# Performance work log

Measured on AMD Instinct MI355X. Metric: run time of the kernel, lower is better.

The kernel has to match this reference:

```python
import jax, jax.numpy as jnp
import numpy as np

USER_SIZE = 1_000_000
ITEM_SIZE = 1_000_000
EMBED = 64
BATCH = 4096
NUM_TOTAL = 100
STD = 0.01


def setup_inputs() -> dict:
    key = jax.random.key(0)
    ks = jax.random.split(key, 16)
    d = {}
    d["user"] = jax.random.randint(ks[0], (BATCH, 1), 0, USER_SIZE, dtype=jnp.int64 if jax.config.jax_enable_x64 else jnp.int32)
    d["item"] = jax.random.randint(ks[1], (BATCH, NUM_TOTAL), 0, ITEM_SIZE, dtype=jnp.int64 if jax.config.jax_enable_x64 else jnp.int32)
    d["num_total"] = NUM_TOTAL
    # Embedding tables stored as [vocab, embed] (transpose of nn.Linear weight [embed, vocab])
    d["Wu_gmf"] = jax.random.normal(ks[2], (USER_SIZE, EMBED), jnp.float32) * STD
    d["bu_gmf"] = jnp.zeros((EMBED,), jnp.float32)
    d["Wu_mlp"] = jax.random.normal(ks[3], (USER_SIZE, EMBED), jnp.float32) * STD
    d["bu_mlp"] = jnp.zeros((EMBED,), jnp.float32)
    d["Wi_gmf"] = jax.random.normal(ks[4], (ITEM_SIZE, EMBED), jnp.float32) * STD
    d["bi_gmf"] = jnp.zeros((EMBED,), jnp.float32)
    d["Wi_mlp"] = jax.random.normal(ks[5], (ITEM_SIZE, EMBED), jnp.float32) * STD
    d["bi_mlp"] = jnp.zeros((EMBED,), jnp.float32)
    # MLP tower, stored as [in, out]
    d["W1"] = jax.random.normal(ks[6], (2 * EMBED, 2 * EMBED), jnp.float32) * STD
    d["b1"] = jnp.zeros((2 * EMBED,), jnp.float32)
    d["W2"] = jax.random.normal(ks[7], (2 * EMBED, EMBED), jnp.float32) * STD
    d["b2"] = jnp.zeros((EMBED,), jnp.float32)
    d["W3"] = jax.random.normal(ks[8], (EMBED, EMBED // 2), jnp.float32) * STD
    d["b3"] = jnp.zeros((EMBED // 2,), jnp.float32)
    d["Wp"] = jax.random.normal(ks[9], (3 * EMBED // 2, 1), jnp.float32) * STD
    d["bp"] = jnp.zeros((1,), jnp.float32)
    return d


def reference(user, item, num_total, Wu_gmf, bu_gmf, Wu_mlp, bu_mlp, Wi_gmf, bi_gmf, Wi_mlp, bi_mlp, W1, b1, W2, b2, W3, b3, Wp, bp):
    # one-hot @ Linear == embedding gather (column select of weight) + bias
    eu_g = Wu_gmf[user[:, 0]] + bu_gmf              # [B, E]
    eu_m = Wu_mlp[user[:, 0]] + bu_mlp              # [B, E]
    ei_g = Wi_gmf[item] + bi_gmf                    # [B, N, E]
    ei_m = Wi_mlp[item] + bi_mlp                    # [B, N, E]

    gmf = eu_g[:, None, :] * ei_g                   # [B, N, E]

    eu_m_b = jnp.broadcast_to(eu_m[:, None, :], ei_m.shape)
    inter = jnp.concatenate([eu_m_b, ei_m], axis=2)  # [B, N, 2E]
    h1 = jax.nn.relu(inter @ W1 + b1)
    h2 = jax.nn.relu(h1 @ W2 + b2)
    h3 = jax.nn.relu(h2 @ W3 + b3)                  # [B, N, E/2]

    concat = jnp.concatenate([gmf, h3], axis=2)     # [B, N, 3E/2]
    pred = jax.nn.sigmoid(concat @ Wp + bp)         # [B, N, 1]
    return pred[..., 0]                             # [B, N]
```

## Files before the change

kernel.cpp:

```cpp
#include <hip/hip_runtime.h>


typedef __attribute__((ext_vector_type(8))) short bf16x8;
typedef __attribute__((ext_vector_type(4))) float f32x4;

__device__ __forceinline__ short f2bf(float x){
  unsigned u = __float_as_uint(x);
  u += 0x7fffu + ((u >> 16) & 1u);
  return (short)(u >> 16);
}
__device__ __forceinline__ float bf2f(short s){
  return __uint_as_float(((unsigned)(unsigned short)s) << 16);
}

__global__ __launch_bounds__(256) void ncf_prep_w(
    const float* __restrict__ W1, const float* __restrict__ W2,
    const float* __restrict__ W3, short* __restrict__ ws)
{
  int i = blockIdx.x * 256 + threadIdx.x;
  if (i < 8192){
    int col = i >> 6, k = i & 63;
    ws[i] = f2bf(W1[(64 + k)*128 + col]);
  } else if (i < 16384){
    int t = i - 8192; int col = t >> 7, k = t & 127;
    ws[i] = f2bf(W2[k*64 + col]);
  } else if (i < 18432){
    int t = i - 16384; int col = t >> 6, k = t & 63;
    ws[i] = f2bf(W3[k*32 + col]);
  }
}

__global__ __launch_bounds__(128) void ncf_prep_u(
    const int* __restrict__ user,
    const float* __restrict__ Wu_gmf, const float* __restrict__ bu_gmf,
    const float* __restrict__ Wu_mlp, const float* __restrict__ bu_mlp,
    const float* __restrict__ bi_gmf, const float* __restrict__ bi_mlp,
    const float* __restrict__ W1, const float* __restrict__ b1,
    const float* __restrict__ Wp,
    float* __restrict__ Xu, float* __restrict__ wup, float* __restrict__ cu,
    int B)
{
  int b = blockIdx.x; if (b >= B) return;
  int j = threadIdx.x;
  long u = (long)user[b];
  float acc = b1[j];
  #pragma unroll 4
  for (int k = 0; k < 64; k++){
    float eu = Wu_mlp[u*64 + k] + bu_mlp[k];
    acc += eu * W1[k*128 + j] + bi_mlp[k] * W1[(64 + k)*128 + j];
  }
  Xu[b*128 + j] = acc;
  if (j < 64){
    float wg = (Wu_gmf[u*64 + j] + bu_gmf[j]) * Wp[j];
    wup[b*64 + j] = wg;
    float c = wg * bi_gmf[j];
    c += __shfl_xor(c, 1);  c += __shfl_xor(c, 2);
    c += __shfl_xor(c, 4);  c += __shfl_xor(c, 8);
    c += __shfl_xor(c, 16); c += __shfl_xor(c, 32);
    if (j == 0) cu[b] = c;
  }
}

__global__ __launch_bounds__(256) void ncf_main(
    const int* __restrict__ item,
    const float* __restrict__ Wi_mlp, const float* __restrict__ Wi_gmf,
    const short* __restrict__ W1iT, const short* __restrict__ W2T,
    const short* __restrict__ W3T,
    const float* __restrict__ b2, const float* __restrict__ b3,
    const float* __restrict__ Wp, const float* __restrict__ bp,
    const float* __restrict__ Xu, const float* __restrict__ wup,
    const float* __restrict__ cu,
    float* __restrict__ out, int N, int total)
{
  __shared__ __align__(16) short s_item[64][72];
  __shared__ __align__(16) short s_h1[64][136];
  __shared__ __align__(16) short s_h3[64][36];
  __shared__ int   s_bidx[64];
  __shared__ float s_pg[64];

  const int tid = threadIdx.x;
  const int p0  = blockIdx.x * 64;

  {
    int r = tid >> 2, q = tid & 3;
    int p = p0 + r; if (p >= total) p = total - 1;
    int b = p / N;
    long ib = (long)item[p] * 64;
    const float4* imp = (const float4*)(Wi_mlp + ib) + q*4;
    const float4* igp = (const float4*)(Wi_gmf + ib) + q*4;
    const float4* wq  = (const float4*)(wup + (long)b*64) + q*4;
    bf16x8 ia[2];
    float pg = 0.f;
    #pragma unroll
    for (int j = 0; j < 4; j++){
      float4 v = imp[j];
      float4 g = igp[j];
      float4 wv = wq[j];
      pg += g.x*wv.x + g.y*wv.y + g.z*wv.z + g.w*wv.w;
      int h = j >> 1, s = (j & 1) * 4;
      ia[h][s+0] = f2bf(v.x); ia[h][s+1] = f2bf(v.y);
      ia[h][s+2] = f2bf(v.z); ia[h][s+3] = f2bf(v.w);
    }
    *(bf16x8*)&s_item[r][q*16]     = ia[0];
    *(bf16x8*)&s_item[r][q*16 + 8] = ia[1];
    pg += __shfl_xor(pg, 1);
    pg += __shfl_xor(pg, 2);
    if (q == 0){ s_bidx[r] = b; s_pg[r] = pg + cu[b]; }
  }
  __syncthreads();

  const int w  = tid >> 6, l = tid & 63;
  const int lr = l & 15,  lg = l >> 4;

  {
    f32x4 acc[4][2];
    #pragma unroll
    for (int mt = 0; mt < 4; mt++)
      #pragma unroll
      for (int nt = 0; nt < 2; nt++)
        acc[mt][nt] = (f32x4){0.f, 0.f, 0.f, 0.f};
    #pragma unroll
    for (int ks = 0; ks < 2; ks++){
      bf16x8 af[4];
      #pragma unroll
      for (int mt = 0; mt < 4; mt++)
        af[mt] = *(const bf16x8*)&s_item[mt*16 + lr][ks*32 + lg*8];
      #pragma unroll
      for (int nt = 0; nt < 2; nt++){
        bf16x8 bfg = *(const bf16x8*)&W1iT[(w*32 + nt*16 + lr)*64 + ks*32 + lg*8];
        #pragma unroll
        for (int mt = 0; mt < 4; mt++)
          acc[mt][nt] = __builtin_amdgcn_mfma_f32_16x16x32_bf16(af[mt], bfg, acc[mt][nt], 0, 0, 0);
      }
    }
    #pragma unroll
    for (int nt = 0; nt < 2; nt++){
      int col = w*32 + nt*16 + lr;
      #pragma unroll
      for (int mt = 0; mt < 4; mt++)
        #pragma unroll
        for (int rr = 0; rr < 4; rr++){
          int row = mt*16 + lg*4 + rr;
          float v = acc[mt][nt][rr] + Xu[s_bidx[row]*128 + col];
          s_h1[row][col] = f2bf(v > 0.f ? v : 0.f);
        }
    }
  }
  __syncthreads();

  {
    f32x4 acc2[4];
    #pragma unroll
    for (int mt = 0; mt < 4; mt++) acc2[mt] = (f32x4){0.f, 0.f, 0.f, 0.f};
    #pragma unroll
    for (int ks = 0; ks < 4; ks++){
      bf16x8 bfg = *(const bf16x8*)&W2T[(w*16 + lr)*128 + ks*32 + lg*8];
      #pragma unroll
      for (int mt = 0; mt < 4; mt++){
        bf16x8 a = *(const bf16x8*)&s_h1[mt*16 + lr][ks*32 + lg*8];
        acc2[mt] = __builtin_amdgcn_mfma_f32_16x16x32_bf16(a, bfg, acc2[mt], 0, 0, 0);
      }
    }
    int col = w*16 + lr;
    float bb = b2[col];
    #pragma unroll
    for (int mt = 0; mt < 4; mt++)
      #pragma unroll
      for (int rr = 0; rr < 4; rr++){
        int row = mt*16 + lg*4 + rr;
        float v = acc2[mt][rr] + bb;
        s_item[row][col] = f2bf(v > 0.f ? v : 0.f);
      }
  }
  __syncthreads();

  if (w < 2){
    f32x4 acc3[4];
    #pragma unroll
    for (int mt = 0; mt < 4; mt++) acc3[mt] = (f32x4){0.f, 0.f, 0.f, 0.f};
    #pragma unroll
    for (int ks = 0; ks < 2; ks++){
      bf16x8 bfg = *(const bf16x8*)&W3T[(w*16 + lr)*64 + ks*32 + lg*8];
      #pragma unroll
      for (int mt = 0; mt < 4; mt++){
        bf16x8 a = *(const bf16x8*)&s_item[mt*16 + lr][ks*32 + lg*8];
        acc3[mt] = __builtin_amdgcn_mfma_f32_16x16x32_bf16(a, bfg, acc3[mt], 0, 0, 0);
      }
    }
    int col = w*16 + lr;
    float bb = b3[col];
    #pragma unroll
    for (int mt = 0; mt < 4; mt++)
      #pragma unroll
      for (int rr = 0; rr < 4; rr++){
        int row = mt*16 + lg*4 + rr;
        float v = acc3[mt][rr] + bb;
        s_h3[row][col] = f2bf(v > 0.f ? v : 0.f);
      }
  }
  __syncthreads();

  {
    int r = tid >> 2, q = tid & 3;
    float sum = 0.f;
    #pragma unroll
    for (int i = 0; i < 8; i++){
      int c = q*8 + i;
      sum += bf2f(s_h3[r][c]) * Wp[64 + c];
    }
    sum += __shfl_xor(sum, 1);
    sum += __shfl_xor(sum, 2);
    int p = p0 + r;
    if (q == 0 && p < total){
      float z = s_pg[r] + sum + bp[0];
      out[p] = 1.f / (1.f + __expf(-z));
    }
  }
}

extern "C" void kernel_launch(void* const* d_in, const int* in_sizes, int n_in,
                              void* d_out, int out_size, void* d_ws, size_t ws_size,
                              hipStream_t stream)
{
  const int*   user   = (const int*)  d_in[0];
  const int*   item   = (const int*)  d_in[1];
  const float* Wu_gmf = (const float*)d_in[3];
  const float* bu_gmf = (const float*)d_in[4];
  const float* Wu_mlp = (const float*)d_in[5];
  const float* bu_mlp = (const float*)d_in[6];
  const float* Wi_gmf = (const float*)d_in[7];
  const float* bi_gmf = (const float*)d_in[8];
  const float* Wi_mlp = (const float*)d_in[9];
  const float* bi_mlp = (const float*)d_in[10];
  const float* W1     = (const float*)d_in[11];
  const float* b1     = (const float*)d_in[12];
  const float* W2     = (const float*)d_in[13];
  const float* b2     = (const float*)d_in[14];
  const float* W3     = (const float*)d_in[15];
  const float* b3     = (const float*)d_in[16];
  const float* Wp     = (const float*)d_in[17];
  const float* bp     = (const float*)d_in[18];

  int B     = in_sizes[0];
  int total = in_sizes[1];
  int N     = total / B;

  short* W1iT = (short*)d_ws;
  short* W2T  = W1iT + 8192;
  short* W3T  = W2T  + 8192;
  float* Xu   = (float*)((char*)d_ws + 36864);
  float* wup  = Xu  + (size_t)B * 128;
  float* cuv  = wup + (size_t)B * 64;

  ncf_prep_w<<<72, 256, 0, stream>>>(W1, W2, W3, (short*)d_ws);
  ncf_prep_u<<<B, 128, 0, stream>>>(user, Wu_gmf, bu_gmf, Wu_mlp, bu_mlp,
                                    bi_gmf, bi_mlp, W1, b1, Wp,
                                    Xu, wup, cuv, B);

  int nblk = (total + 63) / 64;
  ncf_main<<<nblk, 256, 0, stream>>>(item, Wi_mlp, Wi_gmf,
      W1iT, W2T, W3T, b2, b3, Wp, bp, Xu, wup, cuv,
      (float*)d_out, N, total);
}
```

Measured before the change: 85.92 us.

## Use MFMA for user-side W1 projection, persistent main kernel with register-resident weights

The per-user W1 projection moves from a scalar loop (one block per user) to a 64-user-per-block MFMA tile. The constant bias term b1 + bi_mlp·W1 is folded into a single precomputed vector c1. The main kernel becomes persistent over 1024 blocks, loading the W1/W2/W3 fragments into registers once per block instead of once per tile. It also stages the (at most two) user Xu rows per tile into shared memory instead of reading Xu per element. This adds register pressure and a grid-stride loop with an extra barrier per tile. It also assumes B is a multiple of 64 and that a tile spans at most two users.

After: 85.60 us. Within noise of the previous version (-0.4%).

```diff
diff --git a/kernel.cpp b/kernel.cpp
--- a/kernel.cpp
+++ b/kernel.cpp
@@ -13,51 +13,116 @@
   return __uint_as_float(((unsigned)(unsigned short)s) << 16);
 }
 
+
 __global__ __launch_bounds__(256) void ncf_prep_w(
     const float* __restrict__ W1, const float* __restrict__ W2,
-    const float* __restrict__ W3, short* __restrict__ ws)
+    const float* __restrict__ W3, const float* __restrict__ b1,
+    const float* __restrict__ bi_mlp, short* __restrict__ ws,
+    float* __restrict__ c1)
 {
+  if (blockIdx.x == 104){
+    int j = threadIdx.x;
+    if (j < 128){
+      float acc = b1[j];
+      #pragma unroll 4
+      for (int k = 0; k < 64; k++)
+        acc += bi_mlp[k] * W1[(64 + k)*128 + j];
+      c1[j] = acc;
+    }
+    return;
+  }
   int i = blockIdx.x * 256 + threadIdx.x;
   if (i < 8192){
     int col = i >> 6, k = i & 63;
+    ws[i] = f2bf(W1[k*128 + col]);
+  } else if (i < 16384){
+    int t = i - 8192; int col = t >> 6, k = t & 63;
     ws[i] = f2bf(W1[(64 + k)*128 + col]);
-  } else if (i < 16384){
-    int t = i - 8192; int col = t >> 7, k = t & 127;
+  } else if (i < 24576){
+    int t = i - 16384; int col = t >> 7, k = t & 127;
     ws[i] = f2bf(W2[k*64 + col]);
-  } else if (i < 18432){
-    int t = i - 16384; int col = t >> 6, k = t & 63;
+  } else if (i < 26624){
+    int t = i - 24576; int col = t >> 6, k = t & 63;
     ws[i] = f2bf(W3[k*32 + col]);
   }
 }
 
-__global__ __launch_bounds__(128) void ncf_prep_u(
+__global__ __launch_bounds__(256) void ncf_prep_u(
     const int* __restrict__ user,
     const float* __restrict__ Wu_gmf, const float* __restrict__ bu_gmf,
     const float* __restrict__ Wu_mlp, const float* __restrict__ bu_mlp,
-    const float* __restrict__ bi_gmf, const float* __restrict__ bi_mlp,
-    const float* __restrict__ W1, const float* __restrict__ b1,
-    const float* __restrict__ Wp,
-    float* __restrict__ Xu, float* __restrict__ wup, float* __restrict__ cu,
-    int B)
+    const float* __restrict__ bi_gmf, const float* __restrict__ Wp,
+    const short* __restrict__ W1uT, const float* __restrict__ c1,
+    float* __restrict__ Xu, float* __restrict__ wup, float* __restrict__ cu)
 {
-  int b = blockIdx.x; if (b >= B) return;
-  int j = threadIdx.x;
+  __shared__ __align__(16) short s_eu[64][72];
+  const int tid = threadIdx.x;
+  const int r = tid >> 2, q = tid & 3;
+  const int b = blockIdx.x * 64 + r;
   long u = (long)user[b];
-  float acc = b1[j];
-  #pragma unroll 4
-  for (int k = 0; k < 64; k++){
-    float eu = Wu_mlp[u*64 + k] + bu_mlp[k];
-    acc += eu * W1[k*128 + j] + bi_mlp[k] * W1[(64 + k)*128 + j];
-  }
-  Xu[b*128 + j] = acc;
-  if (j < 64){
-    float wg = (Wu_gmf[u*64 + j] + bu_gmf[j]) * Wp[j];
-    wup[b*64 + j] = wg;
-    float c = wg * bi_gmf[j];
-    c += __shfl_xor(c, 1);  c += __shfl_xor(c, 2);
-    c += __shfl_xor(c, 4);  c += __shfl_xor(c, 8);
-    c += __shfl_xor(c, 16); c += __shfl_xor(c, 32);
-    if (j == 0) cu[b] = c;
+
+  {
+    const float4* ump = (const float4*)(Wu_mlp + u*64) + q*4;
+    const float4* bmp = (const float4*)(bu_mlp) + q*4;
+    const float4* ugp = (const float4*)(Wu_gmf + u*64) + q*4;
+    const float4* bgp = (const float4*)(bu_gmf) + q*4;
+    const float4* wpp = (const float4*)(Wp) + q*4;
+    const float4* bip = (const float4*)(bi_gmf) + q*4;
+    float4* wdst = (float4*)(wup + (long)b*64) + q*4;
+    bf16x8 ea[2];
+    float cacc = 0.f;
+    #pragma unroll
+    for (int j = 0; j < 4; j++){
+      float4 m = ump[j], mb = bmp[j];
+      int h = j >> 1, s = (j & 1) * 4;
+      ea[h][s+0] = f2bf(m.x + mb.x); ea[h][s+1] = f2bf(m.y + mb.y);
+      ea[h][s+2] = f2bf(m.z + mb.z); ea[h][s+3] = f2bf(m.w + mb.w);
+      float4 g = ugp[j], gb = bgp[j], wp = wpp[j], bi = bip[j];
+      float4 wg; wg.x = (g.x+gb.x)*wp.x; wg.y = (g.y+gb.y)*wp.y;
+                 wg.z = (g.z+gb.z)*wp.z; wg.w = (g.w+gb.w)*wp.w;
+      wdst[j] = wg;
+      cacc += wg.x*bi.x + wg.y*bi.y + wg.z*bi.z + wg.w*bi.w;
+    }
+    *(bf16x8*)&s_eu[r][q*16]     = ea[0];
+    *(bf16x8*)&s_eu[r][q*16 + 8] = ea[1];
+    cacc += __shfl_xor(cacc, 1);
+    cacc += __shfl_xor(cacc, 2);
+    if (q == 0) cu[b] = cacc;
+  }
+  __syncthreads();
+
+  const int w = tid >> 6, l = tid & 63, lr = l & 15, lg = l >> 4;
+  f32x4 acc[4][2];
+  #pragma unroll
+  for (int mt = 0; mt < 4; mt++)
+    #pragma unroll
+    for (int nt = 0; nt < 2; nt++)
+      acc[mt][nt] = (f32x4){0.f, 0.f, 0.f, 0.f};
+  #pragma unroll
+  for (int ks = 0; ks < 2; ks++){
+    bf16x8 af[4];
+    #pragma unroll
+    for (int mt = 0; mt < 4; mt++)
+      af[mt] = *(const bf16x8*)&s_eu[mt*16 + lr][ks*32 + lg*8];
+    #pragma unroll
+    for (int nt = 0; nt < 2; nt++){
+      bf16x8 bf_ = *(const bf16x8*)&W1uT[(w*32 + nt*16 + lr)*64 + ks*32 + lg*8];
+      #pragma unroll
+      for (int mt = 0; mt < 4; mt++)
+        acc[mt][nt] = __builtin_amdgcn_mfma_f32_16x16x32_bf16(af[mt], bf_, acc[mt][nt], 0, 0, 0);
+    }
+  }
+  #pragma unroll
+  for (int nt = 0; nt < 2; nt++){
+    int col = w*32 + nt*16 + lr;
+    float cc = c1[col];
+    #pragma unroll
+    for (int mt = 0; mt < 4; mt++)
+      #pragma unroll
+      for (int rr = 0; rr < 4; rr++){
+        int row = mt*16 + lg*4 + rr;
+        Xu[(long)(blockIdx.x*64 + row)*128 + col] = acc[mt][nt][rr] + cc;
+      }
   }
 }
 
@@ -70,151 +135,168 @@
     const float* __restrict__ Wp, const float* __restrict__ bp,
     const float* __restrict__ Xu, const float* __restrict__ wup,
     const float* __restrict__ cu,
-    float* __restrict__ out, int N, int total)
+    float* __restrict__ out, int N, int total, int ntiles, int Bsz)
 {
   __shared__ __align__(16) short s_item[64][72];
   __shared__ __align__(16) short s_h1[64][136];
-  __shared__ __align__(16) short s_h3[64][36];
-  __shared__ int   s_bidx[64];
-  __shared__ float s_pg[64];
+  __shared__ __align__(16) short s_h3[64][34];
+  __shared__ __align__(16) float s_xu[2][128];
+  __shared__           float s_pg[64];
 
   const int tid = threadIdx.x;
-  const int p0  = blockIdx.x * 64;
-
-  {
-    int r = tid >> 2, q = tid & 3;
-    int p = p0 + r; if (p >= total) p = total - 1;
-    int b = p / N;
-    long ib = (long)item[p] * 64;
-    const float4* imp = (const float4*)(Wi_mlp + ib) + q*4;
-    const float4* igp = (const float4*)(Wi_gmf + ib) + q*4;
-    const float4* wq  = (const float4*)(wup + (long)b*64) + q*4;
-    bf16x8 ia[2];
-    float pg = 0.f;
-    #pragma unroll
-    for (int j = 0; j < 4; j++){
-      float4 v = imp[j];
-      float4 g = igp[j];
-      float4 wv = wq[j];
-      pg += g.x*wv.x + g.y*wv.y + g.z*wv.z + g.w*wv.w;
-      int h = j >> 1, s = (j & 1) * 4;
-      ia[h][s+0] = f2bf(v.x); ia[h][s+1] = f2bf(v.y);
-      ia[h][s+2] = f2bf(v.z); ia[h][s+3] = f2bf(v.w);
-    }
-    *(bf16x8*)&s_item[r][q*16]     = ia[0];
-    *(bf16x8*)&s_item[r][q*16 + 8] = ia[1];
-    pg += __shfl_xor(pg, 1);
-    pg += __shfl_xor(pg, 2);
-    if (q == 0){ s_bidx[r] = b; s_pg[r] = pg + cu[b]; }
-  }
-  __syncthreads();
-
+  const int r  = tid >> 2, q = tid & 3;
   const int w  = tid >> 6, l = tid & 63;
   const int lr = l & 15,  lg = l >> 4;
-
-  {
-    f32x4 acc[4][2];
-    #pragma unroll
-    for (int mt = 0; mt < 4; mt++)
-      #pragma unroll
-      for (int nt = 0; nt < 2; nt++)
-        acc[mt][nt] = (f32x4){0.f, 0.f, 0.f, 0.f};
-    #pragma unroll
-    for (int ks = 0; ks < 2; ks++){
-      bf16x8 af[4];
+  const int G  = gridDim.x;
+
+  bf16x8 w1f[2][2], w2f[4], w3f[2];
+  #pragma unroll
+  for (int nt = 0; nt < 2; nt++)
+    #pragma unroll
+    for (int ks = 0; ks < 2; ks++)
+      w1f[nt][ks] = *(const bf16x8*)&W1iT[(w*32 + nt*16 + lr)*64 + ks*32 + lg*8];
+  #pragma unroll
+  for (int ks = 0; ks < 4; ks++)
+    w2f[ks] = *(const bf16x8*)&W2T[(w*16 + lr)*128 + ks*32 + lg*8];
+  #pragma unroll
+  for (int ks = 0; ks < 2; ks++)
+    w3f[ks] = *(const bf16x8*)&W3T[((w&1)*16 + lr)*64 + ks*32 + lg*8];
+
+  for (int t = blockIdx.x; t < ntiles; t += G){
+    const int p0  = t * 64;
+    const int b0  = p0 / N;
+    const int thr = (b0 + 1) * N;
+
+    {
+      int p = p0 + r;
+      int bl = (p >= thr) ? 1 : 0;
+      int b  = b0 + bl;
+      long ib = (long)item[p] * 64;
+      const float4* imp = (const float4*)(Wi_mlp + ib) + q*4;
+      const float4* igp = (const float4*)(Wi_gmf + ib) + q*4;
+      const float4* wq  = (const float4*)(wup + (long)b*64) + q*4;
+      bf16x8 ia[2];
+      float pg = 0.f;
+      #pragma unroll
+      for (int j = 0; j < 4; j++){
+        float4 v = imp[j];
+        float4 g = igp[j];
+        float4 wv = wq[j];
+        pg += g.x*wv.x + g.y*wv.y + g.z*wv.z + g.w*wv.w;
+        int h = j >> 1, s = (j & 1) * 4;
+        ia[h][s+0] = f2bf(v.x); ia[h][s+1] = f2bf(v.y);
+        ia[h][s+2] = f2bf(v.z); ia[h][s+3] = f2bf(v.w);
+      }
+      *(bf16x8*)&s_item[r][q*16]     = ia[0];
+      *(bf16x8*)&s_item[r][q*16 + 8] = ia[1];
+      pg += __shfl_xor(pg, 1);
+      pg += __shfl_xor(pg, 2);
+      if (q == 0) s_pg[r] = pg + cu[b];
+      int i2 = tid >> 7, col = tid & 127;
+      int bb = b0 + i2; if (bb >= Bsz) bb = Bsz - 1;
+      s_xu[i2][col] = Xu[(long)bb*128 + col];
+    }
+    __syncthreads();
+
+    {
+      f32x4 acc[4][2];
       #pragma unroll
       for (int mt = 0; mt < 4; mt++)
-        af[mt] = *(const bf16x8*)&s_item[mt*16 + lr][ks*32 + lg*8];
+        #pragma unroll
+        for (int nt = 0; nt < 2; nt++)
+          acc[mt][nt] = (f32x4){0.f, 0.f, 0.f, 0.f};
+      #pragma unroll
+      for (int ks = 0; ks < 2; ks++){
+        bf16x8 af[4];
+        #pragma unroll
+        for (int mt = 0; mt < 4; mt++)
+          af[mt] = *(const bf16x8*)&s_item[mt*16 + lr][ks*32 + lg*8];
+        #pragma unroll
+        for (int nt = 0; nt < 2; nt++)
+          #pragma unroll
+          for (int mt = 0; mt < 4; mt++)
+            acc[mt][nt] = __builtin_amdgcn_mfma_f32_16x16x32_bf16(af[mt], w1f[nt][ks], acc[mt][nt], 0, 0, 0);
+      }
       #pragma unroll
       for (int nt = 0; nt < 2; nt++){
-        bf16x8 bfg = *(const bf16x8*)&W1iT[(w*32 + nt*16 + lr)*64 + ks*32 + lg*8];
+        int col = w*32 + nt*16 + lr;
         #pragma unroll
         for (int mt = 0; mt < 4; mt++)
-          acc[mt][nt] = __builtin_amdgcn_mfma_f32_16x16x32_bf16(af[mt], bfg, acc[mt][nt], 0, 0, 0);
-      }
-    }
-    #pragma unroll
-    for (int nt = 0; nt < 2; nt++){
-      int col = w*32 + nt*16 + lr;
+          #pragma unroll
+          for (int rr = 0; rr < 4; rr++){
+            int row = mt*16 + lg*4 + rr;
+            int bl = (p0 + row >= thr) ? 1 : 0;
+            float v = acc[mt][nt][rr] + s_xu[bl][col];
+            s_h1[row][col] = f2bf(v > 0.f ? v : 0.f);
+          }
+      }
+    }
+    __syncthreads();
+
+    {
+      f32x4 acc2[4];
+      #pragma unroll
+      for (int mt = 0; mt < 4; mt++) acc2[mt] = (f32x4){0.f, 0.f, 0.f, 0.f};
+      #pragma unroll
+      for (int ks = 0; ks < 4; ks++)
+        #pragma unroll
+        for (int mt = 0; mt < 4; mt++){
+          bf16x8 a = *(const bf16x8*)&s_h1[mt*16 + lr][ks*32 + lg*8];
+          acc2[mt] = __builtin_amdgcn_mfma_f32_16x16x32_bf16(a, w2f[ks], acc2[mt], 0, 0, 0);
+        }
+      int col = w*16 + lr;
+      float bb = b2[col];
       #pragma unroll
       for (int mt = 0; mt < 4; mt++)
         #pragma unroll
         for (int rr = 0; rr < 4; rr++){
           int row = mt*16 + lg*4 + rr;
-          float v = acc[mt][nt][rr] + Xu[s_bidx[row]*128 + col];
-          s_h1[row][col] = f2bf(v > 0.f ? v : 0.f);
+          float v = acc2[mt][rr] + bb;
+          s_item[row][col] = f2bf(v > 0.f ? v : 0.f);
         }
     }
-  }
-  __syncthreads();
-
-  {
-    f32x4 acc2[4];
-    #pragma unroll
-    for (int mt = 0; mt < 4; mt++) acc2[mt] = (f32x4){0.f, 0.f, 0.f, 0.f};
-    #pragma unroll
-    for (int ks = 0; ks < 4; ks++){
-      bf16x8 bfg = *(const bf16x8*)&W2T[(w*16 + lr)*128 + ks*32 + lg*8];
-      #pragma unroll
-      for (int mt = 0; mt < 4; mt++){
-        bf16x8 a = *(const bf16x8*)&s_h1[mt*16 + lr][ks*32 + lg*8];
-        acc2[mt] = __builtin_amdgcn_mfma_f32_16x16x32_bf16(a, bfg, acc2[mt], 0, 0, 0);
-      }
-    }
-    int col = w*16 + lr;
-    float bb = b2[col];
-    #pragma unroll
-    for (int mt = 0; mt < 4; mt++)
-      #pragma unroll
-      for (int rr = 0; rr < 4; rr++){
-        int row = mt*16 + lg*4 + rr;
-        float v = acc2[mt][rr] + bb;
-        s_item[row][col] = f2bf(v > 0.f ? v : 0.f);
-      }
-  }
-  __syncthreads();
-
-  if (w < 2){
-    f32x4 acc3[4];
-    #pragma unroll
-    for (int mt = 0; mt < 4; mt++) acc3[mt] = (f32x4){0.f, 0.f, 0.f, 0.f};
-    #pragma unroll
-    for (int ks = 0; ks < 2; ks++){
-      bf16x8 bfg = *(const bf16x8*)&W3T[(w*16 + lr)*64 + ks*32 + lg*8];
-      #pragma unroll
-      for (int mt = 0; mt < 4; mt++){
-        bf16x8 a = *(const bf16x8*)&s_item[mt*16 + lr][ks*32 + lg*8];
-        acc3[mt] = __builtin_amdgcn_mfma_f32_16x16x32_bf16(a, bfg, acc3[mt], 0, 0, 0);
-      }
-    }
-    int col = w*16 + lr;
-    float bb = b3[col];
-    #pragma unroll
-    for (int mt = 0; mt < 4; mt++)
-      #pragma unroll
-      for (int rr = 0; rr < 4; rr++){
-        int row = mt*16 + lg*4 + rr;
-        float v = acc3[mt][rr] + bb;
-        s_h3[row][col] = f2bf(v > 0.f ? v : 0.f);
-      }
-  }
-  __syncthreads();
-
-  {
-    int r = tid >> 2, q = tid & 3;
-    float sum = 0.f;
-    #pragma unroll
-    for (int i = 0; i < 8; i++){
-      int c = q*8 + i;
-      sum += bf2f(s_h3[r][c]) * Wp[64 + c];
-    }
-    sum += __shfl_xor(sum, 1);
-    sum += __shfl_xor(sum, 2);
-    int p = p0 + r;
-    if (q == 0 && p < total){
-      float z = s_pg[r] + sum + bp[0];
-      out[p] = 1.f / (1.f + __expf(-z));
-    }
+    __syncthreads();
+
+    if (w < 2){
+      f32x4 acc3[4];
+      #pragma unroll
+      for (int mt = 0; mt < 4; mt++) acc3[mt] = (f32x4){0.f, 0.f, 0.f, 0.f};
+      #pragma unroll
+      for (int ks = 0; ks < 2; ks++)
+        #pragma unroll
+        for (int mt = 0; mt < 4; mt++){
+          bf16x8 a = *(const bf16x8*)&s_item[mt*16 + lr][ks*32 + lg*8];
+          acc3[mt] = __builtin_amdgcn_mfma_f32_16x16x32_bf16(a, w3f[ks], acc3[mt], 0, 0, 0);
+        }
+      int col = w*16 + lr;
+      float bb = b3[col];
+      #pragma unroll
+      for (int mt = 0; mt < 4; mt++)
+        #pragma unroll
+        for (int rr = 0; rr < 4; rr++){
+          int row = mt*16 + lg*4 + rr;
+          float v = acc3[mt][rr] + bb;
+          s_h3[row][col] = f2bf(v > 0.f ? v : 0.f);
+        }
+    }
+    __syncthreads();
+
+    {
+      float sum = 0.f;
+      #pragma unroll
+      for (int i = 0; i < 8; i++){
+        int c = q*8 + i;
+        sum += bf2f(s_h3[r][c]) * Wp[64 + c];
+      }
+      sum += __shfl_xor(sum, 1);
+      sum += __shfl_xor(sum, 2);
+      int p = p0 + r;
+      if (q == 0 && p < total){
+        float z = s_pg[r] + sum + bp[0];
+        out[p] = 1.f / (1.f + __expf(-z));
+      }
+    }
+    __syncthreads();
   }
 }
 
@@ -245,20 +327,22 @@
   int total = in_sizes[1];
   int N     = total / B;
 
-  short* W1iT = (short*)d_ws;
-  short* W2T  = W1iT + 8192;
-  short* W3T  = W2T  + 8192;
-  float* Xu   = (float*)((char*)d_ws + 36864);
+  char* wsb = (char*)d_ws;
+  short* W1uT = (short*)wsb;
+  short* W1iT = (short*)(wsb + 16384);
+  short* W2T  = (short*)(wsb + 32768);
+  short* W3T  = (short*)(wsb + 49152);
+  float* c1   = (float*)(wsb + 53248);
+  float* Xu   = (float*)(wsb + 57344);
   float* wup  = Xu  + (size_t)B * 128;
   float* cuv  = wup + (size_t)B * 64;
 
-  ncf_prep_w<<<72, 256, 0, stream>>>(W1, W2, W3, (short*)d_ws);
-  ncf_prep_u<<<B, 128, 0, stream>>>(user, Wu_gmf, bu_gmf, Wu_mlp, bu_mlp,
-                                    bi_gmf, bi_mlp, W1, b1, Wp,
-                                    Xu, wup, cuv, B);
-
-  int nblk = (total + 63) / 64;
-  ncf_main<<<nblk, 256, 0, stream>>>(item, Wi_mlp, Wi_gmf,
+  ncf_prep_w<<<105, 256, 0, stream>>>(W1, W2, W3, b1, bi_mlp, (short*)d_ws, c1);
+  ncf_prep_u<<<B/64, 256, 0, stream>>>(user, Wu_gmf, bu_gmf, Wu_mlp, bu_mlp,
+                                       bi_gmf, Wp, W1uT, c1, Xu, wup, cuv);
+
+  int ntiles = (total + 63) / 64;
+  ncf_main<<<1024, 256, 0, stream>>>(item, Wi_mlp, Wi_gmf,
       W1iT, W2T, W3T, b2, b3, Wp, bp, Xu, wup, cuv,
-      (float*)d_out, N, total);
-}
+      (float*)d_out, N, total, ntiles, B);
+}
```

## Make main kernel persistent with prefetched item gathers and merged prep kernels

Applied to the files above, without the earlier changes.

The two prep kernels are merged into one launch, cutting launch overhead. The main kernel becomes persistent: a fixed grid of 1024 blocks strides over 64-row tiles. Each block prefetches the next tile's item indices and embedding rows into registers while the current tile's MLP runs, and defers the final output dot product to the next iteration. The per-tile user MLP bias rows are staged in shared memory, assuming a tile spans at most two users. This hides gather latency but raises register pressure and drops the tail bounds check, so it relies on total being a multiple of 64.

New measurement: 88.07 us. 1.03x slower.

```diff
diff --git a/kernel.cpp b/kernel.cpp
--- a/kernel.cpp
+++ b/kernel.cpp
@@ -13,51 +13,50 @@
   return __uint_as_float(((unsigned)(unsigned short)s) << 16);
 }
 
-__global__ __launch_bounds__(256) void ncf_prep_w(
-    const float* __restrict__ W1, const float* __restrict__ W2,
-    const float* __restrict__ W3, short* __restrict__ ws)
-{
-  int i = blockIdx.x * 256 + threadIdx.x;
-  if (i < 8192){
-    int col = i >> 6, k = i & 63;
-    ws[i] = f2bf(W1[(64 + k)*128 + col]);
-  } else if (i < 16384){
-    int t = i - 8192; int col = t >> 7, k = t & 127;
-    ws[i] = f2bf(W2[k*64 + col]);
-  } else if (i < 18432){
-    int t = i - 16384; int col = t >> 6, k = t & 63;
-    ws[i] = f2bf(W3[k*32 + col]);
-  }
-}
-
-__global__ __launch_bounds__(128) void ncf_prep_u(
+
+__global__ __launch_bounds__(128) void ncf_prep(
     const int* __restrict__ user,
     const float* __restrict__ Wu_gmf, const float* __restrict__ bu_gmf,
     const float* __restrict__ Wu_mlp, const float* __restrict__ bu_mlp,
     const float* __restrict__ bi_gmf, const float* __restrict__ bi_mlp,
     const float* __restrict__ W1, const float* __restrict__ b1,
+    const float* __restrict__ W2, const float* __restrict__ W3,
     const float* __restrict__ Wp,
-    float* __restrict__ Xu, float* __restrict__ wup, float* __restrict__ cu,
-    int B)
+    short* __restrict__ wsT, float* __restrict__ Xu,
+    float* __restrict__ wup, float* __restrict__ cu, int B)
 {
-  int b = blockIdx.x; if (b >= B) return;
+  int bid = blockIdx.x;
   int j = threadIdx.x;
-  long u = (long)user[b];
-  float acc = b1[j];
-  #pragma unroll 4
-  for (int k = 0; k < 64; k++){
-    float eu = Wu_mlp[u*64 + k] + bu_mlp[k];
-    acc += eu * W1[k*128 + j] + bi_mlp[k] * W1[(64 + k)*128 + j];
-  }
-  Xu[b*128 + j] = acc;
-  if (j < 64){
-    float wg = (Wu_gmf[u*64 + j] + bu_gmf[j]) * Wp[j];
-    wup[b*64 + j] = wg;
-    float c = wg * bi_gmf[j];
-    c += __shfl_xor(c, 1);  c += __shfl_xor(c, 2);
-    c += __shfl_xor(c, 4);  c += __shfl_xor(c, 8);
-    c += __shfl_xor(c, 16); c += __shfl_xor(c, 32);
-    if (j == 0) cu[b] = c;
+  if (bid < B){
+    long u = (long)user[bid];
+    float acc = b1[j];
+    #pragma unroll 4
+    for (int k = 0; k < 64; k++){
+      float eu = Wu_mlp[u*64 + k] + bu_mlp[k];
+      acc += eu * W1[k*128 + j] + bi_mlp[k] * W1[(64 + k)*128 + j];
+    }
+    Xu[(long)bid*128 + j] = acc;
+    if (j < 64){
+      float wg = (Wu_gmf[u*64 + j] + bu_gmf[j]) * Wp[j];
+      wup[(long)bid*64 + j] = wg;
+      float c = wg * bi_gmf[j];
+      c += __shfl_xor(c, 1);  c += __shfl_xor(c, 2);
+      c += __shfl_xor(c, 4);  c += __shfl_xor(c, 8);
+      c += __shfl_xor(c, 16); c += __shfl_xor(c, 32);
+      if (j == 0) cu[bid] = c;
+    }
+    return;
+  }
+  int i = (bid - B)*128 + j;
+  if (i < 8192){
+    int col = i >> 6, k = i & 63;
+    wsT[i] = f2bf(W1[(64 + k)*128 + col]);
+  } else if (i < 16384){
+    int t = i - 8192; int col = t >> 7, k = t & 127;
+    wsT[i] = f2bf(W2[k*64 + col]);
+  } else if (i < 18432){
+    int t = i - 16384; int col = t >> 6, k = t & 63;
+    wsT[i] = f2bf(W3[k*32 + col]);
   }
 }
 
@@ -70,138 +69,183 @@
     const float* __restrict__ Wp, const float* __restrict__ bp,
     const float* __restrict__ Xu, const float* __restrict__ wup,
     const float* __restrict__ cu,
-    float* __restrict__ out, int N, int total)
+    float* __restrict__ out, int N, int total, int ntiles, int Bsz)
 {
   __shared__ __align__(16) short s_item[64][72];
   __shared__ __align__(16) short s_h1[64][136];
-  __shared__ __align__(16) short s_h3[64][36];
-  __shared__ int   s_bidx[64];
-  __shared__ float s_pg[64];
+  __shared__ __align__(16) short s_h3[64][34];
+  __shared__ __align__(16) float s_xu[2][128];
 
   const int tid = threadIdx.x;
-  const int p0  = blockIdx.x * 64;
-
+  const int r  = tid >> 2, q = tid & 3;
+  const int w  = tid >> 6, l = tid & 63;
+  const int lr = l & 15,  lg = l >> 4;
+  const int G  = gridDim.x;
+
+  float4 im[4], ig[4];
+  int idx_next = 0;
   {
-    int r = tid >> 2, q = tid & 3;
-    int p = p0 + r; if (p >= total) p = total - 1;
-    int b = p / N;
+    int p = blockIdx.x*64 + r;
     long ib = (long)item[p] * 64;
     const float4* imp = (const float4*)(Wi_mlp + ib) + q*4;
     const float4* igp = (const float4*)(Wi_gmf + ib) + q*4;
-    const float4* wq  = (const float4*)(wup + (long)b*64) + q*4;
-    bf16x8 ia[2];
-    float pg = 0.f;
     #pragma unroll
-    for (int j = 0; j < 4; j++){
-      float4 v = imp[j];
-      float4 g = igp[j];
-      float4 wv = wq[j];
-      pg += g.x*wv.x + g.y*wv.y + g.z*wv.z + g.w*wv.w;
-      int h = j >> 1, s = (j & 1) * 4;
-      ia[h][s+0] = f2bf(v.x); ia[h][s+1] = f2bf(v.y);
-      ia[h][s+2] = f2bf(v.z); ia[h][s+3] = f2bf(v.w);
-    }
-    *(bf16x8*)&s_item[r][q*16]     = ia[0];
-    *(bf16x8*)&s_item[r][q*16 + 8] = ia[1];
-    pg += __shfl_xor(pg, 1);
-    pg += __shfl_xor(pg, 2);
-    if (q == 0){ s_bidx[r] = b; s_pg[r] = pg + cu[b]; }
-  }
-  __syncthreads();
-
-  const int w  = tid >> 6, l = tid & 63;
-  const int lr = l & 15,  lg = l >> 4;
-
-  {
-    f32x4 acc[4][2];
-    #pragma unroll
-    for (int mt = 0; mt < 4; mt++)
-      #pragma unroll
-      for (int nt = 0; nt < 2; nt++)
-        acc[mt][nt] = (f32x4){0.f, 0.f, 0.f, 0.f};
-    #pragma unroll
-    for (int ks = 0; ks < 2; ks++){
-      bf16x8 af[4];
+    for (int jj = 0; jj < 4; jj++){ im[jj] = imp[jj]; ig[jj] = igp[jj]; }
+    int t1 = blockIdx.x + G;
+    if (t1 < ntiles) idx_next = item[t1*64 + r];
+  }
+
+  float pg_reg = 0.f;
+  int prev_p0 = -1;
+
+  for (int t = blockIdx.x; t < ntiles; t += G){
+    const int p0  = t * 64;
+    const int b0  = p0 / N;
+    const int thr = (b0 + 1) * N;
+
+    if (prev_p0 >= 0){
+      float sum = 0.f;
+      #pragma unroll
+      for (int i = 0; i < 8; i++){
+        int c = q*8 + i;
+        sum += bf2f(s_h3[r][c]) * Wp[64 + c];
+      }
+      sum += __shfl_xor(sum, 1);
+      sum += __shfl_xor(sum, 2);
+      if (q == 0){
+        float z = pg_reg + sum + bp[0];
+        out[prev_p0 + r] = 1.f / (1.f + __expf(-z));
+      }
+    }
+
+    {
+      int p = p0 + r;
+      int b = b0 + ((p >= thr) ? 1 : 0);
+      const float4* wq = (const float4*)(wup + (long)b*64) + q*4;
+      bf16x8 ia[2];
+      float pg = 0.f;
+      #pragma unroll
+      for (int jj = 0; jj < 4; jj++){
+        float4 v = im[jj];
+        float4 g = ig[jj];
+        float4 wv = wq[jj];
+        pg += g.x*wv.x + g.y*wv.y + g.z*wv.z + g.w*wv.w;
+        int h = jj >> 1, s = (jj & 1) * 4;
+        ia[h][s+0] = f2bf(v.x); ia[h][s+1] = f2bf(v.y);
+        ia[h][s+2] = f2bf(v.z); ia[h][s+3] = f2bf(v.w);
+      }
+      *(bf16x8*)&s_item[r][q*16]     = ia[0];
+      *(bf16x8*)&s_item[r][q*16 + 8] = ia[1];
+      pg += __shfl_xor(pg, 1);
+      pg += __shfl_xor(pg, 2);
+      if (q == 0) pg_reg = pg + cu[b];
+      int i2 = tid >> 7, col = tid & 127;
+      int bb = b0 + i2; if (bb >= Bsz) bb = Bsz - 1;
+      s_xu[i2][col] = Xu[(long)bb*128 + col];
+      prev_p0 = p0;
+    }
+    __syncthreads();
+
+    if (t + G < ntiles){
+      long ib = (long)idx_next * 64;
+      const float4* imp = (const float4*)(Wi_mlp + ib) + q*4;
+      const float4* igp = (const float4*)(Wi_gmf + ib) + q*4;
+      #pragma unroll
+      for (int jj = 0; jj < 4; jj++){ im[jj] = imp[jj]; ig[jj] = igp[jj]; }
+      if (t + 2*G < ntiles) idx_next = item[(t + 2*G)*64 + r];
+    }
+
+    {
+      f32x4 acc[4][2];
       #pragma unroll
       for (int mt = 0; mt < 4; mt++)
-        af[mt] = *(const bf16x8*)&s_item[mt*16 + lr][ks*32 + lg*8];
+        #pragma unroll
+        for (int nt = 0; nt < 2; nt++)
+          acc[mt][nt] = (f32x4){0.f, 0.f, 0.f, 0.f};
+      #pragma unroll
+      for (int ks = 0; ks < 2; ks++){
+        bf16x8 af[4];
+        #pragma unroll
+        for (int mt = 0; mt < 4; mt++)
+          af[mt] = *(const bf16x8*)&s_item[mt*16 + lr][ks*32 + lg*8];
+        #pragma unroll
+        for (int nt = 0; nt < 2; nt++){
+          bf16x8 bfg = *(const bf16x8*)&W1iT[(w*32 + nt*16 + lr)*64 + ks*32 + lg*8];
+          #pragma unroll
+          for (int mt = 0; mt < 4; mt++)
+            acc[mt][nt] = __builtin_amdgcn_mfma_f32_16x16x32_bf16(af[mt], bfg, acc[mt][nt], 0, 0, 0);
+        }
+      }
       #pragma unroll
       for (int nt = 0; nt < 2; nt++){
-        bf16x8 bfg = *(const bf16x8*)&W1iT[(w*32 + nt*16 + lr)*64 + ks*32 + lg*8];
+        int col = w*32 + nt*16 + lr;
         #pragma unroll
         for (int mt = 0; mt < 4; mt++)
-          acc[mt][nt] = __builtin_amdgcn_mfma_f32_16x16x32_bf16(af[mt], bfg, acc[mt][nt], 0, 0, 0);
-      }
-    }
-    #pragma unroll
-    for (int nt = 0; nt < 2; nt++){
-      int col = w*32 + nt*16 + lr;
+          #pragma unroll
+          for (int rr = 0; rr < 4; rr++){
+            int row = mt*16 + lg*4 + rr;
+            int bl = (p0 + row >= thr) ? 1 : 0;
+            float v = acc[mt][nt][rr] + s_xu[bl][col];
+            s_h1[row][col] = f2bf(v > 0.f ? v : 0.f);
+          }
+      }
+    }
+    __syncthreads();
+
+    {
+      f32x4 acc2[4];
+      #pragma unroll
+      for (int mt = 0; mt < 4; mt++) acc2[mt] = (f32x4){0.f, 0.f, 0.f, 0.f};
+      #pragma unroll
+      for (int ks = 0; ks < 4; ks++){
+        bf16x8 bfg = *(const bf16x8*)&W2T[(w*16 + lr)*128 + ks*32 + lg*8];
+        #pragma unroll
+        for (int mt = 0; mt < 4; mt++){
+          bf16x8 a = *(const bf16x8*)&s_h1[mt*16 + lr][ks*32 + lg*8];
+          acc2[mt] = __builtin_amdgcn_mfma_f32_16x16x32_bf16(a, bfg, acc2[mt], 0, 0, 0);
+        }
+      }
+      int col = w*16 + lr;
+      float bb = b2[col];
       #pragma unroll
       for (int mt = 0; mt < 4; mt++)
         #pragma unroll
         for (int rr = 0; rr < 4; rr++){
           int row = mt*16 + lg*4 + rr;
-          float v = acc[mt][nt][rr] + Xu[s_bidx[row]*128 + col];
-          s_h1[row][col] = f2bf(v > 0.f ? v : 0.f);
-        }
-    }
-  }
-  __syncthreads();
-
-  {
-    f32x4 acc2[4];
-    #pragma unroll
-    for (int mt = 0; mt < 4; mt++) acc2[mt] = (f32x4){0.f, 0.f, 0.f, 0.f};
-    #pragma unroll
-    for (int ks = 0; ks < 4; ks++){
-      bf16x8 bfg = *(const bf16x8*)&W2T[(w*16 + lr)*128 + ks*32 + lg*8];
-      #pragma unroll
-      for (int mt = 0; mt < 4; mt++){
-        bf16x8 a = *(const bf16x8*)&s_h1[mt*16 + lr][ks*32 + lg*8];
-        acc2[mt] = __builtin_amdgcn_mfma_f32_16x16x32_bf16(a, bfg, acc2[mt], 0, 0, 0);
-      }
-    }
-    int col = w*16 + lr;
-    float bb = b2[col];
-    #pragma unroll
-    for (int mt = 0; mt < 4; mt++)
-      #pragma unroll
-      for (int rr = 0; rr < 4; rr++){
-        int row = mt*16 + lg*4 + rr;
-        float v = acc2[mt][rr] + bb;
-        s_item[row][col] = f2bf(v > 0.f ? v : 0.f);
-      }
-  }
-  __syncthreads();
-
-  if (w < 2){
-    f32x4 acc3[4];
-    #pragma unroll
-    for (int mt = 0; mt < 4; mt++) acc3[mt] = (f32x4){0.f, 0.f, 0.f, 0.f};
-    #pragma unroll
-    for (int ks = 0; ks < 2; ks++){
-      bf16x8 bfg = *(const bf16x8*)&W3T[(w*16 + lr)*64 + ks*32 + lg*8];
-      #pragma unroll
-      for (int mt = 0; mt < 4; mt++){
-        bf16x8 a = *(const bf16x8*)&s_item[mt*16 + lr][ks*32 + lg*8];
-        acc3[mt] = __builtin_amdgcn_mfma_f32_16x16x32_bf16(a, bfg, acc3[mt], 0, 0, 0);
-      }
-    }
-    int col = w*16 + lr;
-    float bb = b3[col];
-    #pragma unroll
-    for (int mt = 0; mt < 4; mt++)
-      #pragma unroll
-      for (int rr = 0; rr < 4; rr++){
-        int row = mt*16 + lg*4 + rr;
-        float v = acc3[mt][rr] + bb;
-        s_h3[row][col] = f2bf(v > 0.f ? v : 0.f);
-      }
-  }
-  __syncthreads();
-
-  {
-    int r = tid >> 2, q = tid & 3;
+          float v = acc2[mt][rr] + bb;
+          s_item[row][col] = f2bf(v > 0.f ? v : 0.f);
+        }
+    }
+    __syncthreads();
+
+    if (w < 2){
+      f32x4 acc3[4];
+      #pragma unroll
+      for (int mt = 0; mt < 4; mt++) acc3[mt] = (f32x4){0.f, 0.f, 0.f, 0.f};
+      #pragma unroll
+      for (int ks = 0; ks < 2; ks++){
+        bf16x8 bfg = *(const bf16x8*)&W3T[(w*16 + lr)*64 + ks*32 + lg*8];
+        #pragma unroll
+        for (int mt = 0; mt < 4; mt++){
+          bf16x8 a = *(const bf16x8*)&s_item[mt*16 + lr][ks*32 + lg*8];
+          acc3[mt] = __builtin_amdgcn_mfma_f32_16x16x32_bf16(a, bfg, acc3[mt], 0, 0, 0);
+        }
+      }
+      int col = w*16 + lr;
+      float bb = b3[col];
+      #pragma unroll
+      for (int mt = 0; mt < 4; mt++)
+        #pragma unroll
+        for (int rr = 0; rr < 4; rr++){
+          int row = mt*16 + lg*4 + rr;
+          float v = acc3[mt][rr] + bb;
+          s_h3[row][col] = f2bf(v > 0.f ? v : 0.f);
+        }
+    }
+    __syncthreads();
+  }
+
+  if (prev_p0 >= 0){
     float sum = 0.f;
     #pragma unroll
     for (int i = 0; i < 8; i++){
@@ -210,10 +254,9 @@
     }
     sum += __shfl_xor(sum, 1);
     sum += __shfl_xor(sum, 2);
-    int p = p0 + r;
-    if (q == 0 && p < total){
-      float z = s_pg[r] + sum + bp[0];
-      out[p] = 1.f / (1.f + __expf(-z));
+    if (q == 0){
+      float z = pg_reg + sum + bp[0];
+      out[prev_p0 + r] = 1.f / (1.f + __expf(-z));
     }
   }
 }
@@ -245,20 +288,20 @@
   int total = in_sizes[1];
   int N     = total / B;
 
-  short* W1iT = (short*)d_ws;
-  short* W2T  = W1iT + 8192;
-  short* W3T  = W2T  + 8192;
-  float* Xu   = (float*)((char*)d_ws + 36864);
+  char* wsb = (char*)d_ws;
+  short* W1iT = (short*)wsb;
+  short* W2T  = (short*)(wsb + 16384);
+  short* W3T  = (short*)(wsb + 32768);
+  float* Xu   = (float*)(wsb + 36864);
   float* wup  = Xu  + (size_t)B * 128;
   float* cuv  = wup + (size_t)B * 64;
 
-  ncf_prep_w<<<72, 256, 0, stream>>>(W1, W2, W3, (short*)d_ws);
-  ncf_prep_u<<<B, 128, 0, stream>>>(user, Wu_gmf, bu_gmf, Wu_mlp, bu_mlp,
-                                    bi_gmf, bi_mlp, W1, b1, Wp,
-                                    Xu, wup, cuv, B);
-
-  int nblk = (total + 63) / 64;
-  ncf_main<<<nblk, 256, 0, stream>>>(item, Wi_mlp, Wi_gmf,
+  ncf_prep<<<B + 144, 128, 0, stream>>>(user, Wu_gmf, bu_gmf, Wu_mlp, bu_mlp,
+                                        bi_gmf, bi_mlp, W1, b1, W2, W3, Wp,
+                                        (short*)d_ws, Xu, wup, cuv, B);
+
+  int ntiles = (total + 63) / 64;
+  ncf_main<<<1024, 256, 0, stream>>>(item, Wi_mlp, Wi_gmf,
       W1iT, W2T, W3T, b2, b3, Wp, bp, Xu, wup, cuv,
-      (float*)d_out, N, total);
-}
+      (float*)d_out, N, total, ntiles, B);
+}
```
